# Performance work log

Measured on AMD Instinct MI355X. Metric: run time of the kernel, lower is better.

## Reference

```python
import jax, jax.numpy as jnp
import numpy as np

# ---- placement DB constants (from init_kwargs) ----
XL, XH, YL, YH = 0.0, 1000.0, 0.0, 1000.0
NBX, NBY = 256, 256
BSX = (XH - XL) / NBX
BSY = (YH - YL) / NBY
UHC, UVC = 1.5625, 1.45           # unit horizontal/vertical routing capacity
MAX_RATE = 2.0
MIN_RATE = 1.0 / MAX_RATE
NUM_NETS = 100000
NUM_NODES = 120000
NUM_MOVABLE = 100000
PINS_PER_NET = 4
NUM_PINS = NUM_NETS * PINS_PER_NET


def setup_inputs() -> dict:
    key = jax.random.key(0)
    k1, k2, k3, k4, k5, k6 = jax.random.split(key, 6)
    # node positions: x block then y block, kept inside the die
    pos_x = jax.random.uniform(k1, (NUM_NODES,), jnp.float32) * (XH - XL - 5.0) + XL
    pos_y = jax.random.uniform(k2, (NUM_NODES,), jnp.float32) * (YH - YL - 5.0) + YL
    pos = jnp.concatenate([pos_x, pos_y])
    # pin positions: x block then y block
    pin_x = jax.random.uniform(k3, (NUM_PINS,), jnp.float32) * (XH - XL) + XL
    pin_y = jax.random.uniform(k4, (NUM_PINS,), jnp.float32) * (YH - YL) + YL
    pin_pos = jnp.concatenate([pin_x, pin_y])
    # node sizes in [1, 5)
    node_size_x = jax.random.uniform(k5, (NUM_NODES,), jnp.float32) * 4.0 + 1.0
    node_size_y = jax.random.uniform(k6, (NUM_NODES,), jnp.float32) * 4.0 + 1.0
    net_weights = jnp.ones((NUM_NETS,), jnp.float32)
    # ragged net->pin CSR: fixed 4 pins per net, randomly permuted pin ids
    netpin_start = jnp.arange(NUM_NETS + 1, dtype=jnp.int64) * PINS_PER_NET
    flat_netpin = jax.random.permutation(jax.random.key(7), NUM_PINS).astype(jnp.int64)
    return {"pos": pos, "pin_pos": pin_pos, "node_size_x": node_size_x,
            "node_size_y": node_size_y, "net_weights": net_weights,
            "netpin_start": netpin_start, "flat_netpin": flat_netpin}


def _overlap_1d(lo, hi, nbins, bl, bs):
    """Overlap length of [lo,hi] intervals with each bin. lo,hi: [N] -> [N, nbins]."""
    bin_lo = bl + bs * jnp.arange(nbins, dtype=lo.dtype)
    bin_hi = bin_lo + bs
    ov = jnp.minimum(hi[:, None], bin_hi[None, :]) - jnp.maximum(lo[:, None], bin_lo[None, :])
    return jnp.maximum(ov, 0.0)


def reference(pos, pin_pos, node_size_x, node_size_y, net_weights, netpin_start, flat_netpin):
    num_pins = pin_pos.shape[0] // 2
    # ---- phase 1: per-net bbox via ragged CSR gather + segment reduce ----
    px = pin_pos[flat_netpin]             # [P] pin x
    py = pin_pos[flat_netpin + num_pins]  # [P] pin y
    seg = jnp.searchsorted(netpin_start[1:], jnp.arange(flat_netpin.shape[0]), side='right')
    xmin = jax.ops.segment_min(px, seg, num_segments=NUM_NETS)
    xmax = jax.ops.segment_max(px, seg, num_segments=NUM_NETS)
    ymin = jax.ops.segment_min(py, seg, num_segments=NUM_NETS)
    ymax = jax.ops.segment_max(py, seg, num_segments=NUM_NETS)
    wx = xmax - xmin
    wy = ymax - ymin
    bbox_area = jnp.maximum(wx * wy, jnp.float32(1e-6))  # guard degenerate nets
    # RUDY demand densities (per unit area inside the bbox)
    h_dens = net_weights * wx / bbox_area  # horizontal demand density
    v_dens = net_weights * wy / bbox_area  # vertical demand density
    # separable bbox-bin overlaps
    ox = _overlap_1d(xmin, xmax, NBX, XL, BSX)  # [N, Bx]
    oy = _overlap_1d(ymin, ymax, NBY, YL, BSY)  # [N, By]
    h_map = jnp.einsum('nx,ny->xy', ox * h_dens[:, None], oy)  # [Bx, By]
    v_map = jnp.einsum('nx,ny->xy', ox * v_dens[:, None], oy)
    h_util = h_map / (BSX * BSY * UHC)
    v_util = v_map / (BSX * BSY * UVC)
    util = jnp.clip(jnp.maximum(h_util, v_util), MIN_RATE, MAX_RATE)
    # ---- phase 2: scatter congestion-weighted area to movable nodes ----
    nx = pos[:NUM_MOVABLE]
    ny = pos[NUM_NODES:NUM_NODES + NUM_MOVABLE]
    sx = node_size_x[:NUM_MOVABLE]
    sy = node_size_y[:NUM_MOVABLE]
    oxn = _overlap_1d(nx, nx + sx, NBX, XL, BSX)  # [M, Bx]
    oyn = _overlap_1d(ny, ny + sy, NBY, YL, BSY)  # [M, By]
    instance_route_area = jnp.einsum('ix,xy,iy->i', oxn, util, oyn)  # [M]
    return instance_route_area
```

## Files before the change

kernel.cpp:

```cpp
#include <hip/hip_runtime.h>


#define NB 256
#define NW 4
#define NWIN 64
#define NCHUNK 16
#define K2_THREADS 512
#define FXS 65536.0f
#define INV_FXS (1.0f / 65536.0f)
#define LCAP 2048
#define LFLUSH 1536
#define MAXSTRIPS 16

__device__ __forceinline__ long long load_idx(const void* p, long long i, int is64) {
    if (is64) return ((const long long*)p)[i];
    return (long long)((const int*)p)[i];
}

__global__ void bbox_kernel(const float* __restrict__ pin_pos,
                            const float* __restrict__ net_weights,
                            const void* __restrict__ netpin_start,
                            const void* __restrict__ flat_netpin,
                            unsigned long long* __restrict__ wmask,
                            float2* __restrict__ yb,
                            float4* __restrict__ rd,
                            int num_nets, int num_pins) {
    int gid = blockIdx.x * blockDim.x + threadIdx.x;
    int n = gid >> 2, k = gid & 3;
    if (n >= num_nets) return;
    const int is64 = (((const int*)netpin_start)[1] == 0);
    long long s = load_idx(netpin_start, n, is64);
    long long e = load_idx(netpin_start, n + 1, is64);
    float xmn = 3e38f, xmx = -3e38f, ymn = 3e38f, ymx = -3e38f;
    if (e - s == 4) {
        long long pin = load_idx(flat_netpin, s + k, is64);
        float px = pin_pos[pin], py = pin_pos[pin + num_pins];
        xmn = px; xmx = px; ymn = py; ymx = py;
    } else if (k == 0) {
        for (long long p = s; p < e; ++p) {
            long long pin = load_idx(flat_netpin, p, is64);
            float px = pin_pos[pin], py = pin_pos[pin + num_pins];
            xmn = fminf(xmn, px); xmx = fmaxf(xmx, px);
            ymn = fminf(ymn, py); ymx = fmaxf(ymx, py);
        }
    }
    #pragma unroll
    for (int m = 1; m <= 2; m <<= 1) {
        xmn = fminf(xmn, __shfl_xor(xmn, m));
        xmx = fmaxf(xmx, __shfl_xor(xmx, m));
        ymn = fminf(ymn, __shfl_xor(ymn, m));
        ymx = fmaxf(ymx, __shfl_xor(ymx, m));
    }
    if (k) return;
    if (e <= s) { wmask[n] = 0ull; return; }
    float wx = xmx - xmn, wy = ymx - ymn;
    float area = fmaxf(wx * wy, 1e-6f);
    float w = net_weights[n];
    const float INVB = 1.0f / 3.90625f;
    int j0 = (int)floorf(ymn * INVB);
    int j1 = (int)floorf(ymx * INVB);
    unsigned long long m = 0ull;
    if ((unsigned)j0 < 256u)       m |= 1ull << (j0 >> 2);
    if ((unsigned)(j0 + 1) < 256u) m |= 1ull << ((j0 + 1) >> 2);
    if ((unsigned)j1 < 256u)       m |= 1ull << (j1 >> 2);
    if ((unsigned)(j1 + 1) < 256u) m |= 1ull << ((j1 + 1) >> 2);
    wmask[n] = m;
    yb[n] = make_float2(ymn, ymx);
    rd[n] = make_float4(xmn, xmx, w * wx / area, w * wy / area);
}

__global__ __launch_bounds__(K2_THREADS) void accum9(
        const unsigned long long* __restrict__ wmask,
        const float2* __restrict__ yb,
        const float4* __restrict__ rd,
        float* __restrict__ PT,
        int num_nets) {
    __shared__ float acc[2 * NW * NB];
    __shared__ int   l_idx[LCAP];
    __shared__ int   lcount;
    int* acci = (int*)acc;
    const int win   = blockIdx.x >> 4;
    const int chunk = blockIdx.x & 15;
    const int r0    = win * NW;
    const int tid   = threadIdx.x;
    const int lane  = tid & 63;
    const float BSX  = 3.90625f;
    const float INVB = 1.0f / 3.90625f;

    for (int i = tid; i < 2 * NW * NB; i += K2_THREADS) acci[i] = 0;
    if (tid == 0) lcount = 0;

    const int c0 = (int)((long long)num_nets * chunk / NCHUNK);
    const int c1 = (int)((long long)num_nets * (chunk + 1) / NCHUNK);
    const int nstrips = (c1 - c0 + K2_THREADS - 1) / K2_THREADS;

    unsigned long long wm[MAXSTRIPS];
    #pragma unroll
    for (int s = 0; s < MAXSTRIPS; ++s) {
        int n = c0 + s * K2_THREADS + tid;
        wm[s] = (s < nstrips && n < c1) ? wmask[n] : 0ull;
    }
    __syncthreads();

    auto flush = [&](int cnt) {
        for (int i = tid; i < cnt; i += K2_THREADS) {
            int n = l_idx[i];
            float2 y = yb[n];
            float4 r = rd[n];
            float ty0 = y.x * INVB, fj0 = floorf(ty0);
            float ty1 = y.y * INVB, fj1 = floorf(ty1);
            int j0 = (int)fj0, j1 = (int)fj1;
            float f0 = ty0 - fj0, f1 = ty1 - fj1;
            float tx0 = r.x * INVB, g0 = floorf(tx0);
            float tx1 = r.y * INVB, g1 = floorf(tx1);
            int i0 = (int)g0, i1 = (int)g1;
            float h0 = tx0 - g0, h1 = tx1 - g1;
            int   xx[4] = { i0, i0 + 1, i1, i1 + 1 };
            float ax[4] = { BSX * (1.f - h0), BSX * h0,
                           -BSX * (1.f - h1), -BSX * h1 };
            int   rr[4] = { j0, j0 + 1, j1, j1 + 1 };
            float rw[4] = { BSX * (1.f - f0), BSX * f0,
                           -BSX * (1.f - f1), -BSX * f1 };
            #pragma unroll
            for (int q = 0; q < 4; ++q) {
                int ro = rr[q] - r0;
                if ((unsigned)ro >= NW) continue;
                float wh = rw[q] * r.z * FXS;
                float wv = rw[q] * r.w * FXS;
                int* bh = acci + ro * NB;
                int* bv = acci + NW * NB + ro * NB;
                #pragma unroll
                for (int p = 0; p < 4; ++p) {
                    int x = xx[p];
                    if (x >= NB) continue;
                    atomicAdd(bh + x, __float2int_rn(ax[p] * wh));
                    atomicAdd(bv + x, __float2int_rn(ax[p] * wv));
                }
            }
        }
    };

    for (int s = 0; s < nstrips; ++s) {
        int n = c0 + s * K2_THREADS + tid;
        bool hit = ((wm[s] >> win) & 1ull) != 0ull;
        unsigned long long m = __ballot(hit);
        if (m) {
            int base = 0;
            if (lane == 0) base = atomicAdd(&lcount, (int)__popcll(m));
            base = __shfl(base, 0);
            if (hit) {
                int pos = base + (int)__popcll(m & ((1ull << lane) - 1ull));
                if (pos < LCAP) l_idx[pos] = n;
            }
        }
        if (s == nstrips - 1 || lcount >= LFLUSH) {
            __syncthreads();
            int cnt = lcount; if (cnt > LCAP) cnt = LCAP;
            flush(cnt);
            __syncthreads();
            if (tid == 0) lcount = 0;
            __syncthreads();
        }
    }

    const int wave = tid >> 6;
    for (int row = wave; row < 2 * NW; row += (K2_THREADS / 64)) {
        float carry = 0.f;
        #pragma unroll
        for (int seg = 0; seg < NB / 64; ++seg) {
            int idx = row * NB + seg * 64 + lane;
            float v = (float)acci[idx] * INV_FXS;
            #pragma unroll
            for (int off = 1; off < 64; off <<= 1) {
                float u = __shfl_up(v, off);
                if (lane >= off) v += u;
            }
            v += carry;
            acc[idx] = v;
            carry = __shfl(v, 63);
        }
    }
    __syncthreads();

    {
        int i = tid;
        int p = i >> 8;
        int x = i & 255;
        int base = p * NW * NB;
        float4 v;
        v.x = acc[base + 0 * NB + x];
        v.y = acc[base + 1 * NB + x];
        v.z = acc[base + 2 * NB + x];
        v.w = acc[base + 3 * NB + x];
        float* dst = PT + ((((long long)chunk * 2 + p) * NB + x) * NB) + r0;
        *(float4*)dst = v;
    }
}

__global__ __launch_bounds__(512) void yscan_util(
        const float* __restrict__ PT, float* __restrict__ utilT) {
    __shared__ float buf[2 * NB];
    const int x = blockIdx.x;
    const int plane = threadIdx.x >> 8;
    const int y = threadIdx.x & (NB - 1);
    float s = 0.f;
    #pragma unroll 8
    for (int c = 0; c < NCHUNK; ++c)
        s += PT[(((long long)c * 2 + plane) * NB + x) * NB + y];
    float* b = buf + plane * NB;
    b[y] = s;
    #pragma unroll
    for (int off = 1; off < NB; off <<= 1) {
        __syncthreads();
        float a = (y >= off) ? b[y - off] : 0.0f;
        __syncthreads();
        b[y] += a;
    }
    __syncthreads();
    if (plane == 0) {
        const float INV_CH = 1.0f / (3.90625f * 3.90625f * 1.5625f);
        const float INV_CV = 1.0f / (3.90625f * 3.90625f * 1.45f);
        float u = fmaxf(buf[y] * INV_CH, buf[NB + y] * INV_CV);
        u = fminf(fmaxf(u, 0.5f), 2.0f);
        utilT[x * NB + y] = u;
    }
}

__global__ void instance_area(const float* __restrict__ pos,
                              const float* __restrict__ nsx,
                              const float* __restrict__ nsy,
                              const float* __restrict__ utilT,
                              float* __restrict__ out,
                              int num_movable, int num_nodes) {
    int i = blockIdx.x * blockDim.x + threadIdx.x;
    if (i >= num_movable) return;
    const float BSX = 3.90625f;
    const float INVB = 1.0f / 3.90625f;
    float x0f = pos[i];
    float y0f = pos[num_nodes + i];
    float x1f = x0f + nsx[i];
    float y1f = y0f + nsy[i];
    int kx0 = max(0, min(NB - 1, (int)floorf(x0f * INVB)));
    int kx1 = max(0, min(NB - 1, (int)floorf(x1f * INVB)));
    int ky0 = max(0, min(NB - 1, (int)floorf(y0f * INVB)));
    int ky1 = max(0, min(NB - 1, (int)floorf(y1f * INVB)));
    float acc = 0.0f;
    for (int kx = kx0; kx <= kx1; ++kx) {
        float bx = kx * BSX;
        float ovx = fmaxf(fminf(x1f, bx + BSX) - fmaxf(x0f, bx), 0.0f);
        const float* ucol = utilT + kx * NB;
        float accy = 0.0f;
        for (int ky = ky0; ky <= ky1; ++ky) {
            float by = ky * BSX;
            float ovy = fmaxf(fminf(y1f, by + BSX) - fmaxf(y0f, by), 0.0f);
            accy += ovy * ucol[ky];
        }
        acc += accy * ovx;
    }
    out[i] = acc;
}

__global__ void fb_zero(float* g, int n) {
    int i = blockIdx.x * blockDim.x + threadIdx.x;
    int stride = gridDim.x * blockDim.x;
    for (; i < n; i += stride) g[i] = 0.0f;
}

__global__ void fb_scatter(const float* __restrict__ pin_pos,
                           const float* __restrict__ net_weights,
                           const void* __restrict__ netpin_start,
                           const void* __restrict__ flat_netpin,
                           float* __restrict__ G2,
                           int num_nets, int num_pins) {
    int n = blockIdx.x * blockDim.x + threadIdx.x;
    if (n >= num_nets) return;
    const int is64 = (((const int*)netpin_start)[1] == 0);
    long long s = load_idx(netpin_start, n, is64);
    long long e = load_idx(netpin_start, n + 1, is64);
    if (e <= s) return;
    float xmn = 3e38f, xmx = -3e38f, ymn = 3e38f, ymx = -3e38f;
    for (long long p = s; p < e; ++p) {
        long long pin = load_idx(flat_netpin, p, is64);
        float px = pin_pos[pin], py = pin_pos[pin + num_pins];
        xmn = fminf(xmn, px); xmx = fmaxf(xmx, px);
        ymn = fminf(ymn, py); ymx = fmaxf(ymx, py);
    }
    float wx = xmx - xmn, wy = ymx - ymn;
    float area = fmaxf(wx * wy, 1e-6f);
    float w = net_weights[n];
    float dh = w * wx / area, dv = w * wy / area;
    const float BSX = 3.90625f, INVB = 1.0f / 3.90625f;
    int jx[4]; float ax[4]; int jy[4]; float ay[4];
    float t, fj, f; int j;
    t = xmn * INVB; fj = floorf(t); j = (int)fj; f = t - fj;
    jx[0] = j; ax[0] = BSX * (1.f - f); jx[1] = j + 1; ax[1] = BSX * f;
    t = xmx * INVB; fj = floorf(t); j = (int)fj; f = t - fj;
    jx[2] = j; ax[2] = -BSX * (1.f - f); jx[3] = j + 1; ax[3] = -BSX * f;
    t = ymn * INVB; fj = floorf(t); j = (int)fj; f = t - fj;
    jy[0] = j; ay[0] = BSX * (1.f - f); jy[1] = j + 1; ay[1] = BSX * f;
    t = ymx * INVB; fj = floorf(t); j = (int)fj; f = t - fj;
    jy[2] = j; ay[2] = -BSX * (1.f - f); jy[3] = j + 1; ay[3] = -BSX * f;
    #pragma unroll
    for (int b = 0; b < 4; ++b) {
        int y = jy[b];
        if (y < 0 || y >= NB) continue;
        #pragma unroll
        for (int a2 = 0; a2 < 4; ++a2) {
            int x = jx[a2];
            if (x < 0 || x >= NB) continue;
            float g = ax[a2] * ay[b];
            atomicAdd(&G2[(y * NB + x) * 2],     dh * g);
            atomicAdd(&G2[(y * NB + x) * 2 + 1], dv * g);
        }
    }
}

__global__ void fb_rowscan(float2* G2) {
    int y = blockIdx.x, t = threadIdx.x;
    __shared__ float sh[NB]; __shared__ float sv[NB];
    float2 v = G2[y * NB + t];
    sh[t] = v.x; sv[t] = v.y;
    #pragma unroll
    for (int off = 1; off < NB; off <<= 1) {
        __syncthreads();
        float a = (t >= off) ? sh[t - off] : 0.0f;
        float b = (t >= off) ? sv[t - off] : 0.0f;
        __syncthreads();
        sh[t] += a; sv[t] += b;
    }
    __syncthreads();
    G2[y * NB + t] = make_float2(sh[t], sv[t]);
}

__global__ void fb_colscan(const float2* __restrict__ G2, float* __restrict__ utilT) {
    int x = blockIdx.x, t = threadIdx.x;
    const float INV_CH = 1.0f / (3.90625f * 3.90625f * 1.5625f);
    const float INV_CV = 1.0f / (3.90625f * 3.90625f * 1.45f);
    __shared__ float sh[NB]; __shared__ float sv[NB];
    float2 g = G2[t * NB + x];
    sh[t] = g.x; sv[t] = g.y;
    #pragma unroll
    for (int off = 1; off < NB; off <<= 1) {
        __syncthreads();
        float a = (t >= off) ? sh[t - off] : 0.0f;
        float b = (t >= off) ? sv[t - off] : 0.0f;
        __syncthreads();
        sh[t] += a; sv[t] += b;
    }
    __syncthreads();
    float u = fmaxf(sh[t] * INV_CH, sv[t] * INV_CV);
    utilT[x * NB + t] = fminf(fmaxf(u, 0.5f), 2.0f);
}

extern "C" void kernel_launch(void* const* d_in, const int* in_sizes, int n_in,
                              void* d_out, int out_size, void* d_ws, size_t ws_size,
                              hipStream_t stream) {
    const float* pos          = (const float*)d_in[0];
    const float* pin_pos      = (const float*)d_in[1];
    const float* nsx          = (const float*)d_in[2];
    const float* nsy          = (const float*)d_in[3];
    const float* net_weights  = (const float*)d_in[4];
    const void*  netpin_start = d_in[5];
    const void*  flat_netpin  = d_in[6];
    float* out = (float*)d_out;

    int num_pins    = in_sizes[1] / 2;
    int num_nodes   = in_sizes[2];
    int num_nets    = in_sizes[4];
    int num_movable = out_size;

    auto align4 = [](size_t v) { return (v + 3) & ~(size_t)3; };
    size_t mk_off = 0;
    size_t yb_off = align4(mk_off + 2LL * num_nets);
    size_t rd_off = align4(yb_off + 2LL * num_nets);
    size_t PT_off = align4(rd_off + 4LL * num_nets);
    size_t PT_f   = (size_t)NCHUNK * 2 * NB * NB;
    size_t ut_off = PT_off + PT_f;
    size_t need   = (ut_off + (size_t)NB * NB) * sizeof(float);

    bool strips_ok = ((num_nets + NCHUNK - 1) / NCHUNK + K2_THREADS - 1) / K2_THREADS
                     <= MAXSTRIPS;

    if (ws_size >= need && strips_ok) {
        float* base = (float*)d_ws;
        unsigned long long* wmask = (unsigned long long*)(base + mk_off);
        float2*   yb    = (float2*)(base + yb_off);
        float4*   rd    = (float4*)(base + rd_off);
        float*    PT    = base + PT_off;
        float*    ut    = base + ut_off;

        int g1 = (4 * num_nets + 255) / 256;
        bbox_kernel<<<g1, 256, 0, stream>>>(pin_pos, net_weights, netpin_start,
                                            flat_netpin, wmask, yb, rd,
                                            num_nets, num_pins);
        accum9<<<NWIN * NCHUNK, K2_THREADS, 0, stream>>>(wmask, yb, rd, PT, num_nets);
        yscan_util<<<NB, 512, 0, stream>>>(PT, ut);
        int gi = (num_movable + 255) / 256;
        instance_area<<<gi, 256, 0, stream>>>(pos, nsx, nsy, ut, out,
                                              num_movable, num_nodes);
        return;
    }

    {
        float* G2   = (float*)d_ws;
        float* util = G2 + NB * NB * 2;
        fb_zero<<<256, 256, 0, stream>>>(G2, NB * NB * 2);
        int gn = (num_nets + 255) / 256;
        fb_scatter<<<gn, 256, 0, stream>>>(pin_pos, net_weights, netpin_start,
                                           flat_netpin, G2, num_nets, num_pins);
        fb_rowscan<<<NB, 256, 0, stream>>>((float2*)G2);
        fb_colscan<<<NB, 256, 0, stream>>>((const float2*)G2, util);
        int gi = (num_movable + 255) / 256;
        instance_area<<<gi, 256, 0, stream>>>(pos, nsx, nsy, util, out,
                                              num_movable, num_nodes);
    }
}
```

Before: 35.72 us.

## Use 1024-thread accumulation blocks with fewer chunks and split H/V planes across threads

The accumulation kernel now runs with 1024 threads per block and 8 net chunks instead of 512 threads and 16 chunks, which halves the partial planes that the y-scan must sum. In the flush step each listed net is handled by two threads, one for the horizontal plane and one for the vertical, to spread the shared-memory atomics. The flush condition is now read after a barrier on every strip, which adds a sync per strip but makes the count check uniform across the block. With fewer, larger blocks, each window has less parallelism and each block performs more LDS atomics.

```diff
diff --git a/kernel.cpp b/kernel.cpp
--- a/kernel.cpp
+++ b/kernel.cpp
@@ -4,12 +4,12 @@
 #define NB 256
 #define NW 4
 #define NWIN 64
-#define NCHUNK 16
-#define K2_THREADS 512
+#define NCHUNK 8
+#define K2_THREADS 1024
 #define FXS 65536.0f
 #define INV_FXS (1.0f / 65536.0f)
 #define LCAP 2048
-#define LFLUSH 1536
+#define LFLUSH 1024
 #define MAXSTRIPS 16
 
 __device__ __forceinline__ long long load_idx(const void* p, long long i, int is64) {
@@ -69,7 +69,7 @@
     rd[n] = make_float4(xmn, xmx, w * wx / area, w * wy / area);
 }
 
-__global__ __launch_bounds__(K2_THREADS) void accum9(
+__global__ __launch_bounds__(K2_THREADS) void accum10(
         const unsigned long long* __restrict__ wmask,
         const float2* __restrict__ yb,
         const float4* __restrict__ rd,
@@ -79,8 +79,8 @@
     __shared__ int   l_idx[LCAP];
     __shared__ int   lcount;
     int* acci = (int*)acc;
-    const int win   = blockIdx.x >> 4;
-    const int chunk = blockIdx.x & 15;
+    const int win   = blockIdx.x >> 3;
+    const int chunk = blockIdx.x & 7;
     const int r0    = win * NW;
     const int tid   = threadIdx.x;
     const int lane  = tid & 63;
@@ -103,7 +103,9 @@
     __syncthreads();
 
     auto flush = [&](int cnt) {
-        for (int i = tid; i < cnt; i += K2_THREADS) {
+        for (int ii = tid; ii < 2 * cnt; ii += K2_THREADS) {
+            int i  = (ii < cnt) ? ii : ii - cnt;
+            int pl = (ii < cnt) ? 0 : 1;
             int n = l_idx[i];
             float2 y = yb[n];
             float4 r = rd[n];
@@ -115,6 +117,8 @@
             float tx1 = r.y * INVB, g1 = floorf(tx1);
             int i0 = (int)g0, i1 = (int)g1;
             float h0 = tx0 - g0, h1 = tx1 - g1;
+            float d = pl ? r.w : r.z;
+            int* bp = acci + pl * (NW * NB);
             int   xx[4] = { i0, i0 + 1, i1, i1 + 1 };
             float ax[4] = { BSX * (1.f - h0), BSX * h0,
                            -BSX * (1.f - h1), -BSX * h1 };
@@ -125,16 +129,13 @@
             for (int q = 0; q < 4; ++q) {
                 int ro = rr[q] - r0;
                 if ((unsigned)ro >= NW) continue;
-                float wh = rw[q] * r.z * FXS;
-                float wv = rw[q] * r.w * FXS;
-                int* bh = acci + ro * NB;
-                int* bv = acci + NW * NB + ro * NB;
+                float wd = rw[q] * d * FXS;
+                int* b2 = bp + ro * NB;
                 #pragma unroll
                 for (int p = 0; p < 4; ++p) {
                     int x = xx[p];
                     if (x >= NB) continue;
-                    atomicAdd(bh + x, __float2int_rn(ax[p] * wh));
-                    atomicAdd(bv + x, __float2int_rn(ax[p] * wv));
+                    atomicAdd(b2 + x, __float2int_rn(ax[p] * wd));
                 }
             }
         }
@@ -153,9 +154,9 @@
                 if (pos < LCAP) l_idx[pos] = n;
             }
         }
-        if (s == nstrips - 1 || lcount >= LFLUSH) {
-            __syncthreads();
-            int cnt = lcount; if (cnt > LCAP) cnt = LCAP;
+        __syncthreads();
+        int cnt = lcount; if (cnt > LCAP) cnt = LCAP;
+        if (cnt >= LFLUSH || s == nstrips - 1) {
             flush(cnt);
             __syncthreads();
             if (tid == 0) lcount = 0;
@@ -182,10 +183,9 @@
     }
     __syncthreads();
 
-    {
-        int i = tid;
-        int p = i >> 8;
-        int x = i & 255;
+    if (tid < 512) {
+        int p = tid >> 8;
+        int x = tid & 255;
         int base = p * NW * NB;
         float4 v;
         v.x = acc[base + 0 * NB + x];
@@ -204,7 +204,7 @@
     const int plane = threadIdx.x >> 8;
     const int y = threadIdx.x & (NB - 1);
     float s = 0.f;
-    #pragma unroll 8
+    #pragma unroll
     for (int c = 0; c < NCHUNK; ++c)
         s += PT[(((long long)c * 2 + plane) * NB + x) * NB + y];
     float* b = buf + plane * NB;
@@ -393,7 +393,7 @@
         bbox_kernel<<<g1, 256, 0, stream>>>(pin_pos, net_weights, netpin_start,
                                             flat_netpin, wmask, yb, rd,
                                             num_nets, num_pins);
-        accum9<<<NWIN * NCHUNK, K2_THREADS, 0, stream>>>(wmask, yb, rd, PT, num_nets);
+        accum10<<<NWIN * NCHUNK, K2_THREADS, 0, stream>>>(wmask, yb, rd, PT, num_nets);
         yscan_util<<<NB, 512, 0, stream>>>(PT, ut);
         int gi = (num_movable + 255) / 256;
         instance_area<<<gi, 256, 0, stream>>>(pos, nsx, nsy, ut, out,
```

Result: no change. 35.05 us (-1.9%).
